# Kernel tuning notes

Hardware: AMD Instinct MI355X
Metric: run time of the kernel (lower is better)

The kernel has to match this reference:

```python
import math
import jax, jax.numpy as jnp
import numpy as np

B, S, E, H = 4, 2048, 2048, 16
D = E // H
EPSILON, DELTA, MAX_GRAD_NORM = 1.0, 1e-05, 1.0
# Gaussian mechanism calibration: sigma = C * sqrt(2 ln(1.25/delta)) / epsilon
NOISE_SCALE = MAX_GRAD_NORM * math.sqrt(2.0 * math.log(1.25 / DELTA)) / EPSILON


def _xavier(key, fan_in, fan_out):
    lim = math.sqrt(6.0 / (fan_in + fan_out))
    return jax.random.uniform(key, (fan_out, fan_in), jnp.float32, -lim, lim)


def setup_inputs() -> dict:
    key = jax.random.key(0)
    ks = jax.random.split(key, 8)
    return {
        'query': jax.random.normal(ks[0], (B, S, E), jnp.float32),
        'key_t': jax.random.normal(ks[1], (B, S, E), jnp.float32),
        'value': jax.random.normal(ks[2], (B, S, E), jnp.float32),
        'Wq': _xavier(ks[3], E, E), 'bq': jnp.zeros((E,), jnp.float32),
        'Wk': _xavier(ks[4], E, E), 'bk': jnp.zeros((E,), jnp.float32),
        'Wv': _xavier(ks[5], E, E), 'bv': jnp.zeros((E,), jnp.float32),
        'Wo': _xavier(ks[6], E, E), 'bo': jnp.zeros((E,), jnp.float32),
        'noise': jax.random.normal(ks[7], (B, S, E), jnp.float32),
    }


def reference(query, key_t, value, Wq, bq, Wk, bk, Wv, bv, Wo, bo, noise):
    b, s, e = query.shape
    scale = 1.0 / math.sqrt(D)
    # QKV projections (torch Linear: x @ W.T + b) -> [b, s, H, D]
    q = (query @ Wq.T + bq).reshape(b, s, H, D)
    k = (key_t @ Wk.T + bk).reshape(b, s, H, D)
    v = (value @ Wv.T + bv).reshape(b, s, H, D)
    # attention scores [b, H, s, s]
    scores = jnp.einsum('bqhd,bkhd->bhqk', q, k) * scale
    attn = jax.nn.softmax(scores, axis=-1)
    ctx = jnp.einsum('bhqk,bkhd->bqhd', attn, v).reshape(b, s, e)
    # DP noise injected inside the kernel on the attention output
    ctx = ctx + noise * NOISE_SCALE
    # output projection
    return ctx @ Wo.T + bo
```

## Files before the change

kernel.cpp:

```cpp
#include <hip/hip_runtime.h>
#include <cmath>

#define BATCH 4
#define SEQ   2048
#define EMB   2048
#define NH    16
#define HD    128
#define MDIM  (BATCH*SEQ)
#define KDIM  EMB
#define NDIM  EMB

typedef __bf16 bf16x8 __attribute__((ext_vector_type(8)));
typedef float  f32x4  __attribute__((ext_vector_type(4)));

__device__ __forceinline__ ushort bf16rne(float f) {
  unsigned u = __builtin_bit_cast(unsigned, f);
  u += 0x7fffu + ((u >> 16) & 1u);
  return (ushort)(u >> 16);
}

__global__ __launch_bounds__(256) void cvt_bf16(const float* __restrict__ in,
                                                ushort* __restrict__ out) {
  int i = (blockIdx.x * 256 + threadIdx.x) * 4;
  float4 v = *(const float4*)(in + i);
  ushort4 o;
  o.x = bf16rne(v.x); o.y = bf16rne(v.y); o.z = bf16rne(v.z); o.w = bf16rne(v.w);
  *(ushort4*)(out + i) = o;
}

template<int MODE>
__global__ __launch_bounds__(256, 2)
void gemm_nt(const ushort* __restrict__ A, const ushort* __restrict__ Bm,
             const float* __restrict__ bias, void* __restrict__ out) {
  __shared__ ushort As[128][72];
  __shared__ ushort Bs[128][72];

  const int tid  = threadIdx.x;
  const int wave = tid >> 6, lane = tid & 63;
  const int l15  = lane & 15, quad = lane >> 4;
  const int m0 = blockIdx.x * 128, n0 = blockIdx.y * 128;
  const int wr = (wave >> 1) * 64, wc = (wave & 1) * 64;

  const f32x4 zero4 = {0.f, 0.f, 0.f, 0.f};
  f32x4 acc[4][4];
#pragma unroll
  for (int i = 0; i < 4; ++i)
#pragma unroll
    for (int j = 0; j < 4; ++j) acc[i][j] = zero4;

  for (int kk = 0; kk < KDIM; kk += 64) {
#pragma unroll
    for (int it = 0; it < 4; ++it) {
      int L = it * 256 + tid;
      int row = L >> 3, c8 = (L & 7) * 8;
      int4 va = *(const int4*)(A  + (size_t)(m0 + row) * KDIM + kk + c8);
      int4 vb = *(const int4*)(Bm + (size_t)(n0 + row) * KDIM + kk + c8);
      *(int4*)(&As[row][c8]) = va;
      *(int4*)(&Bs[row][c8]) = vb;
    }
    __syncthreads();
#pragma unroll
    for (int ks = 0; ks < 2; ++ks) {
      bf16x8 af[4], bfr[4];
#pragma unroll
      for (int i = 0; i < 4; ++i)
        af[i] = __builtin_bit_cast(bf16x8, *(const int4*)(&As[wr + i*16 + l15][ks*32 + quad*8]));
#pragma unroll
      for (int j = 0; j < 4; ++j)
        bfr[j] = __builtin_bit_cast(bf16x8, *(const int4*)(&Bs[wc + j*16 + l15][ks*32 + quad*8]));
#pragma unroll
      for (int i = 0; i < 4; ++i)
#pragma unroll
        for (int j = 0; j < 4; ++j)
          acc[i][j] = __builtin_amdgcn_mfma_f32_16x16x32_bf16(af[i], bfr[j], acc[i][j], 0, 0, 0);
    }
    __syncthreads();
  }

  if constexpr (MODE == 0) {
    float* O = (float*)out;
#pragma unroll
    for (int i = 0; i < 4; ++i)
#pragma unroll
      for (int j = 0; j < 4; ++j) {
        int n = n0 + wc + j*16 + l15;
        float bb = bias[n];
#pragma unroll
        for (int r = 0; r < 4; ++r) {
          int m = m0 + wr + i*16 + quad*4 + r;
          O[(size_t)m * NDIM + n] = acc[i][j][r] + bb;
        }
      }
  } else if constexpr (MODE == 1) {
    ushort* O = (ushort*)out;
#pragma unroll
    for (int i = 0; i < 4; ++i)
#pragma unroll
      for (int j = 0; j < 4; ++j) {
        int n = n0 + wc + j*16 + l15;
        float bb = bias[n];
        int h = n >> 7, d = n & 127;
#pragma unroll
        for (int r = 0; r < 4; ++r) {
          int m = m0 + wr + i*16 + quad*4 + r;
          int b = m >> 11, srow = m & 2047;
          O[(((size_t)(b*NH + h) * SEQ + srow) << 7) + d] = bf16rne(acc[i][j][r] + bb);
        }
      }
  } else {
    __shared__ float Tt[4][16][17];
    ushort* O = (ushort*)out;
    const int h = n0 >> 7;
#pragma unroll
    for (int i = 0; i < 4; ++i)
#pragma unroll
      for (int j = 0; j < 4; ++j) {
        int n = n0 + wc + j*16 + l15;
        float bb = bias[n];
#pragma unroll
        for (int r = 0; r < 4; ++r)
          Tt[wave][l15][quad*4 + r] = acc[i][j][r] + bb;
#pragma unroll
        for (int r = 0; r < 4; ++r) {
          int dl = quad*4 + r, sl = l15;
          float v = Tt[wave][dl][sl];
          int m = m0 + wr + i*16 + sl;
          int b = m >> 11, srow = m & 2047;
          int d = wc + j*16 + dl;
          O[((size_t)(b*NH + h) * HD + d) * SEQ + srow] = bf16rne(v);
        }
      }
  }
}

__global__ __launch_bounds__(256, 2)
void attn_kernel(const ushort* __restrict__ Qh, const ushort* __restrict__ Kh,
                 const ushort* __restrict__ Vt, const float* __restrict__ noise,
                 ushort* __restrict__ ctxn, float scale, float ns) {
  __shared__ ushort Ks[64][136];
  __shared__ ushort Vs[128][72];
  __shared__ ushort Ps[64][72];

  const int tid  = threadIdx.x;
  const int wave = tid >> 6, lane = tid & 63;
  const int l15  = lane & 15, quad = lane >> 4;
  const int q0 = blockIdx.x * 64;
  const int bh = blockIdx.y;
  const int b  = bh >> 4, h = bh & 15;

  bf16x8 qf[4];
  {
    const int qrow = q0 + wave*16 + l15;
    const ushort* qp = Qh + ((size_t)bh * SEQ + qrow) * HD;
#pragma unroll
    for (int ks = 0; ks < 4; ++ks)
      qf[ks] = __builtin_bit_cast(bf16x8, *(const int4*)(qp + ks*32 + quad*8));
  }

  const f32x4 zero4 = {0.f, 0.f, 0.f, 0.f};
  f32x4 o[8];
#pragma unroll
  for (int nb = 0; nb < 8; ++nb) o[nb] = zero4;
  float rs[4] = {0.f, 0.f, 0.f, 0.f};

  for (int k0 = 0; k0 < SEQ; k0 += 64) {
#pragma unroll
    for (int it = 0; it < 4; ++it) {
      int L = it * 256 + tid;
      int r = L >> 4, c8 = (L & 15) * 8;
      *(int4*)(&Ks[r][c8]) = *(const int4*)(Kh + ((size_t)bh * SEQ + k0 + r) * HD + c8);
    }
#pragma unroll
    for (int it = 0; it < 4; ++it) {
      int L = it * 256 + tid;
      int r = L >> 3, c8 = (L & 7) * 8;
      *(int4*)(&Vs[r][c8]) = *(const int4*)(Vt + ((size_t)bh * HD + r) * SEQ + k0 + c8);
    }
    __syncthreads();

#pragma unroll
    for (int ct = 0; ct < 4; ++ct) {
      f32x4 s = zero4;
#pragma unroll
      for (int ks = 0; ks < 4; ++ks) {
        bf16x8 kf = __builtin_bit_cast(bf16x8, *(const int4*)(&Ks[ct*16 + l15][ks*32 + quad*8]));
        s = __builtin_amdgcn_mfma_f32_16x16x32_bf16(qf[ks], kf, s, 0, 0, 0);
      }
#pragma unroll
      for (int r = 0; r < 4; ++r) {
        float p = __expf(s[r] * scale);
        rs[r] += p;
        Ps[wave*16 + quad*4 + r][ct*16 + l15] = bf16rne(p);
      }
    }

#pragma unroll
    for (int ks2 = 0; ks2 < 2; ++ks2) {
      bf16x8 pa = __builtin_bit_cast(bf16x8, *(const int4*)(&Ps[wave*16 + l15][ks2*32 + quad*8]));
#pragma unroll
      for (int nb = 0; nb < 8; ++nb) {
        bf16x8 vb = __builtin_bit_cast(bf16x8, *(const int4*)(&Vs[nb*16 + l15][ks2*32 + quad*8]));
        o[nb] = __builtin_amdgcn_mfma_f32_16x16x32_bf16(pa, vb, o[nb], 0, 0, 0);
      }
    }
    __syncthreads();
  }

#pragma unroll
  for (int r = 0; r < 4; ++r) {
    float v = rs[r];
    v += __shfl_xor(v, 1);
    v += __shfl_xor(v, 2);
    v += __shfl_xor(v, 4);
    v += __shfl_xor(v, 8);
    rs[r] = v;
  }

#pragma unroll
  for (int r = 0; r < 4; ++r) {
    float inv = 1.0f / rs[r];
    int sg = q0 + wave*16 + quad*4 + r;
    size_t rowbase = ((size_t)(b * SEQ + sg)) * EMB + h * HD;
#pragma unroll
    for (int nb = 0; nb < 8; ++nb) {
      int e = nb*16 + l15;
      float val = o[nb][r] * inv + noise[rowbase + e] * ns;
      ctxn[rowbase + e] = bf16rne(val);
    }
  }
}

extern "C" void kernel_launch(void* const* d_in, const int* in_sizes, int n_in,
                              void* d_out, int out_size, void* d_ws, size_t ws_size,
                              hipStream_t stream) {
  const float* query = (const float*)d_in[0];
  const float* key_t = (const float*)d_in[1];
  const float* value = (const float*)d_in[2];
  const float* Wq = (const float*)d_in[3];
  const float* bq = (const float*)d_in[4];
  const float* Wk = (const float*)d_in[5];
  const float* bk = (const float*)d_in[6];
  const float* Wv = (const float*)d_in[7];
  const float* bv = (const float*)d_in[8];
  const float* Wo = (const float*)d_in[9];
  const float* bo = (const float*)d_in[10];
  const float* noise = (const float*)d_in[11];

  const size_t SZ_ACT = (size_t)MDIM * KDIM * 2;
  const size_t SZ_W   = (size_t)NDIM * KDIM * 2;
  const size_t need_full = 7 * SZ_ACT + 4 * SZ_W;

  char* p = (char*)d_ws;
  ushort *qb, *kb;
  if (ws_size >= need_full) {
    qb = (ushort*)p; p += SZ_ACT;
    kb = (ushort*)p; p += SZ_ACT;
  } else {
    qb = (ushort*)d_out;
    kb = (ushort*)((char*)d_out + SZ_ACT);
  }
  ushort* vb   = (ushort*)p; p += SZ_ACT;
  ushort* wqb  = (ushort*)p; p += SZ_W;
  ushort* wkb  = (ushort*)p; p += SZ_W;
  ushort* wvb  = (ushort*)p; p += SZ_W;
  ushort* wob  = (ushort*)p; p += SZ_W;
  ushort* Qh   = (ushort*)p; p += SZ_ACT;
  ushort* Kh   = (ushort*)p; p += SZ_ACT;
  ushort* Vt   = (ushort*)p; p += SZ_ACT;
  ushort* ctxn = (ushort*)p; p += SZ_ACT;

  const int nAct = MDIM * KDIM;
  const int nW   = NDIM * KDIM;
  const float NS = (float)sqrt(2.0 * log(1.25 / 1e-5));
  const float SCALE = (float)(1.0 / sqrt((double)HD));

  cvt_bf16<<<dim3(nAct / 1024), dim3(256), 0, stream>>>(query, qb);
  cvt_bf16<<<dim3(nAct / 1024), dim3(256), 0, stream>>>(key_t, kb);
  cvt_bf16<<<dim3(nAct / 1024), dim3(256), 0, stream>>>(value, vb);
  cvt_bf16<<<dim3(nW / 1024),   dim3(256), 0, stream>>>(Wq, wqb);
  cvt_bf16<<<dim3(nW / 1024),   dim3(256), 0, stream>>>(Wk, wkb);
  cvt_bf16<<<dim3(nW / 1024),   dim3(256), 0, stream>>>(Wv, wvb);
  cvt_bf16<<<dim3(nW / 1024),   dim3(256), 0, stream>>>(Wo, wob);

  dim3 ggrid(MDIM / 128, NDIM / 128);
  gemm_nt<1><<<ggrid, dim3(256), 0, stream>>>(qb, wqb, bq, (void*)Qh);
  gemm_nt<1><<<ggrid, dim3(256), 0, stream>>>(kb, wkb, bk, (void*)Kh);
  gemm_nt<2><<<ggrid, dim3(256), 0, stream>>>(vb, wvb, bv, (void*)Vt);

  attn_kernel<<<dim3(SEQ / 64, BATCH * NH), dim3(256), 0, stream>>>(
      Qh, Kh, Vt, noise, ctxn, SCALE, NS);

  gemm_nt<0><<<ggrid, dim3(256), 0, stream>>>(ctxn, wob, bo, d_out);
}
```

Before: 875.8 us.

## Use direct global-to-LDS loads and double query rows per attention block

Global-to-register-to-LDS staging in both the GEMM and attention kernels is replaced with global_load_lds direct transfers. This drops the padded LDS layouts, so the MFMA operand reads can now hit bank conflicts. The attention kernel also processes 128 query rows per block instead of 64, so each K/V tile loaded into LDS is reused across twice as many queries. The cost is more registers for the doubled accumulators and half as many attention blocks.

```diff
diff --git a/kernel.cpp b/kernel.cpp
--- a/kernel.cpp
+++ b/kernel.cpp
@@ -13,6 +13,10 @@
 typedef __bf16 bf16x8 __attribute__((ext_vector_type(8)));
 typedef float  f32x4  __attribute__((ext_vector_type(4)));
 
+#define GLDS16(gp, lp) \
+  __builtin_amdgcn_global_load_lds((const __attribute__((address_space(1))) void*)(gp), \
+                                   (__attribute__((address_space(3))) void*)(lp), 16, 0, 0)
+
 __device__ __forceinline__ ushort bf16rne(float f) {
   unsigned u = __builtin_bit_cast(unsigned, f);
   u += 0x7fffu + ((u >> 16) & 1u);
@@ -32,8 +36,8 @@
 __global__ __launch_bounds__(256, 2)
 void gemm_nt(const ushort* __restrict__ A, const ushort* __restrict__ Bm,
              const float* __restrict__ bias, void* __restrict__ out) {
-  __shared__ ushort As[128][72];
-  __shared__ ushort Bs[128][72];
+  __shared__ __attribute__((aligned(16))) ushort As[128 * 64];
+  __shared__ __attribute__((aligned(16))) ushort Bs[128 * 64];
 
   const int tid  = threadIdx.x;
   const int wave = tid >> 6, lane = tid & 63;
@@ -41,6 +45,19 @@
   const int m0 = blockIdx.x * 128, n0 = blockIdx.y * 128;
   const int wr = (wave >> 1) * 64, wc = (wave & 1) * 64;
 
+  const ushort* ag[4]; const ushort* bg[4];
+  ushort* la[4]; ushort* lb[4];
+#pragma unroll
+  for (int c = 0; c < 4; ++c) {
+    int ci  = wave * 4 + c;
+    int row = ci * 8 + (lane >> 3);
+    int col = (lane & 7) * 8;
+    ag[c] = A  + (size_t)(m0 + row) * KDIM + col;
+    bg[c] = Bm + (size_t)(n0 + row) * KDIM + col;
+    la[c] = &As[ci * 512];
+    lb[c] = &Bs[ci * 512];
+  }
+
   const f32x4 zero4 = {0.f, 0.f, 0.f, 0.f};
   f32x4 acc[4][4];
 #pragma unroll
@@ -50,13 +67,10 @@
 
   for (int kk = 0; kk < KDIM; kk += 64) {
 #pragma unroll
-    for (int it = 0; it < 4; ++it) {
-      int L = it * 256 + tid;
-      int row = L >> 3, c8 = (L & 7) * 8;
-      int4 va = *(const int4*)(A  + (size_t)(m0 + row) * KDIM + kk + c8);
-      int4 vb = *(const int4*)(Bm + (size_t)(n0 + row) * KDIM + kk + c8);
-      *(int4*)(&As[row][c8]) = va;
-      *(int4*)(&Bs[row][c8]) = vb;
+    for (int c = 0; c < 4; ++c) {
+      GLDS16(ag[c], la[c]);
+      GLDS16(bg[c], lb[c]);
+      ag[c] += 64; bg[c] += 64;
     }
     __syncthreads();
 #pragma unroll
@@ -64,10 +78,10 @@
       bf16x8 af[4], bfr[4];
 #pragma unroll
       for (int i = 0; i < 4; ++i)
-        af[i] = __builtin_bit_cast(bf16x8, *(const int4*)(&As[wr + i*16 + l15][ks*32 + quad*8]));
+        af[i] = __builtin_bit_cast(bf16x8, *(const int4*)(&As[(wr + i*16 + l15) * 64 + ks*32 + quad*8]));
 #pragma unroll
       for (int j = 0; j < 4; ++j)
-        bfr[j] = __builtin_bit_cast(bf16x8, *(const int4*)(&Bs[wc + j*16 + l15][ks*32 + quad*8]));
+        bfr[j] = __builtin_bit_cast(bf16x8, *(const int4*)(&Bs[(wc + j*16 + l15) * 64 + ks*32 + quad*8]));
 #pragma unroll
       for (int i = 0; i < 4; ++i)
 #pragma unroll
@@ -137,95 +151,115 @@
 void attn_kernel(const ushort* __restrict__ Qh, const ushort* __restrict__ Kh,
                  const ushort* __restrict__ Vt, const float* __restrict__ noise,
                  ushort* __restrict__ ctxn, float scale, float ns) {
-  __shared__ ushort Ks[64][136];
-  __shared__ ushort Vs[128][72];
-  __shared__ ushort Ps[64][72];
+  __shared__ __attribute__((aligned(16))) ushort Ks[64 * 128];
+  __shared__ __attribute__((aligned(16))) ushort Vs[128 * 64];
+  __shared__ ushort Ps[128][72];
 
   const int tid  = threadIdx.x;
   const int wave = tid >> 6, lane = tid & 63;
   const int l15  = lane & 15, quad = lane >> 4;
-  const int q0 = blockIdx.x * 64;
+  const int q0 = blockIdx.x * 128;
   const int bh = blockIdx.y;
   const int b  = bh >> 4, h = bh & 15;
 
-  bf16x8 qf[4];
-  {
-    const int qrow = q0 + wave*16 + l15;
+  bf16x8 qf[2][4];
+#pragma unroll
+  for (int s = 0; s < 2; ++s) {
+    const int qrow = q0 + s*64 + wave*16 + l15;
     const ushort* qp = Qh + ((size_t)bh * SEQ + qrow) * HD;
 #pragma unroll
     for (int ks = 0; ks < 4; ++ks)
-      qf[ks] = __builtin_bit_cast(bf16x8, *(const int4*)(qp + ks*32 + quad*8));
+      qf[s][ks] = __builtin_bit_cast(bf16x8, *(const int4*)(qp + ks*32 + quad*8));
+  }
+
+  const ushort* kg[4]; const ushort* vg[4];
+  ushort* lk[4]; ushort* lv[4];
+#pragma unroll
+  for (int c = 0; c < 4; ++c) {
+    int ci = wave * 4 + c;
+    int kr = ci * 4 + (lane >> 4);
+    kg[c] = Kh + ((size_t)bh * SEQ + kr) * HD + (lane & 15) * 8;
+    lk[c] = &Ks[ci * 512];
+    int vr = ci * 8 + (lane >> 3);
+    vg[c] = Vt + ((size_t)bh * HD + vr) * SEQ + (lane & 7) * 8;
+    lv[c] = &Vs[ci * 512];
   }
 
   const f32x4 zero4 = {0.f, 0.f, 0.f, 0.f};
-  f32x4 o[8];
-#pragma unroll
-  for (int nb = 0; nb < 8; ++nb) o[nb] = zero4;
-  float rs[4] = {0.f, 0.f, 0.f, 0.f};
+  f32x4 o[2][8];
+#pragma unroll
+  for (int s = 0; s < 2; ++s)
+#pragma unroll
+    for (int nb = 0; nb < 8; ++nb) o[s][nb] = zero4;
+  float rs[2][4] = {{0.f,0.f,0.f,0.f},{0.f,0.f,0.f,0.f}};
 
   for (int k0 = 0; k0 < SEQ; k0 += 64) {
 #pragma unroll
-    for (int it = 0; it < 4; ++it) {
-      int L = it * 256 + tid;
-      int r = L >> 4, c8 = (L & 15) * 8;
-      *(int4*)(&Ks[r][c8]) = *(const int4*)(Kh + ((size_t)bh * SEQ + k0 + r) * HD + c8);
-    }
-#pragma unroll
-    for (int it = 0; it < 4; ++it) {
-      int L = it * 256 + tid;
-      int r = L >> 3, c8 = (L & 7) * 8;
-      *(int4*)(&Vs[r][c8]) = *(const int4*)(Vt + ((size_t)bh * HD + r) * SEQ + k0 + c8);
+    for (int c = 0; c < 4; ++c) {
+      GLDS16(kg[c], lk[c]);
+      GLDS16(vg[c], lv[c]);
+      kg[c] += (size_t)64 * HD;
+      vg[c] += 64;
     }
     __syncthreads();
 
 #pragma unroll
-    for (int ct = 0; ct < 4; ++ct) {
-      f32x4 s = zero4;
-#pragma unroll
-      for (int ks = 0; ks < 4; ++ks) {
-        bf16x8 kf = __builtin_bit_cast(bf16x8, *(const int4*)(&Ks[ct*16 + l15][ks*32 + quad*8]));
-        s = __builtin_amdgcn_mfma_f32_16x16x32_bf16(qf[ks], kf, s, 0, 0, 0);
-      }
-#pragma unroll
-      for (int r = 0; r < 4; ++r) {
-        float p = __expf(s[r] * scale);
-        rs[r] += p;
-        Ps[wave*16 + quad*4 + r][ct*16 + l15] = bf16rne(p);
-      }
-    }
+    for (int s = 0; s < 2; ++s)
+#pragma unroll
+      for (int ct = 0; ct < 4; ++ct) {
+        f32x4 sc = zero4;
+#pragma unroll
+        for (int ks = 0; ks < 4; ++ks) {
+          bf16x8 kf = __builtin_bit_cast(bf16x8, *(const int4*)(&Ks[(ct*16 + l15) * 128 + ks*32 + quad*8]));
+          sc = __builtin_amdgcn_mfma_f32_16x16x32_bf16(qf[s][ks], kf, sc, 0, 0, 0);
+        }
+#pragma unroll
+        for (int r = 0; r < 4; ++r) {
+          float p = __expf(sc[r] * scale);
+          rs[s][r] += p;
+          Ps[s*64 + wave*16 + quad*4 + r][ct*16 + l15] = bf16rne(p);
+        }
+      }
 
 #pragma unroll
     for (int ks2 = 0; ks2 < 2; ++ks2) {
-      bf16x8 pa = __builtin_bit_cast(bf16x8, *(const int4*)(&Ps[wave*16 + l15][ks2*32 + quad*8]));
+      bf16x8 vb[8];
+#pragma unroll
+      for (int nb = 0; nb < 8; ++nb)
+        vb[nb] = __builtin_bit_cast(bf16x8, *(const int4*)(&Vs[(nb*16 + l15) * 64 + ks2*32 + quad*8]));
+#pragma unroll
+      for (int s = 0; s < 2; ++s) {
+        bf16x8 pa = __builtin_bit_cast(bf16x8, *(const int4*)(&Ps[s*64 + wave*16 + l15][ks2*32 + quad*8]));
+#pragma unroll
+        for (int nb = 0; nb < 8; ++nb)
+          o[s][nb] = __builtin_amdgcn_mfma_f32_16x16x32_bf16(pa, vb[nb], o[s][nb], 0, 0, 0);
+      }
+    }
+    __syncthreads();
+  }
+
+#pragma unroll
+  for (int s = 0; s < 2; ++s) {
+#pragma unroll
+    for (int r = 0; r < 4; ++r) {
+      float v = rs[s][r];
+      v += __shfl_xor(v, 1);
+      v += __shfl_xor(v, 2);
+      v += __shfl_xor(v, 4);
+      v += __shfl_xor(v, 8);
+      rs[s][r] = v;
+    }
+#pragma unroll
+    for (int r = 0; r < 4; ++r) {
+      float inv = 1.0f / rs[s][r];
+      int sg = q0 + s*64 + wave*16 + quad*4 + r;
+      size_t rowbase = ((size_t)(b * SEQ + sg)) * EMB + h * HD;
 #pragma unroll
       for (int nb = 0; nb < 8; ++nb) {
-        bf16x8 vb = __builtin_bit_cast(bf16x8, *(const int4*)(&Vs[nb*16 + l15][ks2*32 + quad*8]));
-        o[nb] = __builtin_amdgcn_mfma_f32_16x16x32_bf16(pa, vb, o[nb], 0, 0, 0);
-      }
-    }
-    __syncthreads();
-  }
-
-#pragma unroll
-  for (int r = 0; r < 4; ++r) {
-    float v = rs[r];
-    v += __shfl_xor(v, 1);
-    v += __shfl_xor(v, 2);
-    v += __shfl_xor(v, 4);
-    v += __shfl_xor(v, 8);
-    rs[r] = v;
-  }
-
-#pragma unroll
-  for (int r = 0; r < 4; ++r) {
-    float inv = 1.0f / rs[r];
-    int sg = q0 + wave*16 + quad*4 + r;
-    size_t rowbase = ((size_t)(b * SEQ + sg)) * EMB + h * HD;
-#pragma unroll
-    for (int nb = 0; nb < 8; ++nb) {
-      int e = nb*16 + l15;
-      float val = o[nb][r] * inv + noise[rowbase + e] * ns;
-      ctxn[rowbase + e] = bf16rne(val);
+        int e = nb*16 + l15;
+        float val = o[s][nb][r] * inv + noise[rowbase + e] * ns;
+        ctxn[rowbase + e] = bf16rne(val);
+      }
     }
   }
 }
@@ -287,7 +321,7 @@
   gemm_nt<1><<<ggrid, dim3(256), 0, stream>>>(kb, wkb, bk, (void*)Kh);
   gemm_nt<2><<<ggrid, dim3(256), 0, stream>>>(vb, wvb, bv, (void*)Vt);
 
-  attn_kernel<<<dim3(SEQ / 64, BATCH * NH), dim3(256), 0, stream>>>(
+  attn_kernel<<<dim3(SEQ / 128, BATCH * NH), dim3(256), 0, stream>>>(
       Qh, Kh, Vt, noise, ctxn, SCALE, NS);
 
   gemm_nt<0><<<ggrid, dim3(256), 0, stream>>>(ctxn, wob, bo, d_out);
```

Measured after the change: 1.114 ms. +27.2%, slower.
